# Kernel tuning notes

Measured on AMD Instinct MI355X. Metric: run time of the kernel, lower is better.

Reference implementation:

```python
import jax, jax.numpy as jnp
import numpy as np

D_MODEL = 1024
GEOM_DIM = 32
CLAMP_VALUE = 10.0


def setup_inputs() -> dict:
    key = jax.random.key(0)
    k1, k2, k3 = jax.random.split(key, 3)
    B, N = 4, 2048
    H = jax.random.normal(k1, (B, N, D_MODEL), dtype=jnp.float32)
    B_prev = jax.random.normal(k2, (B, N, N), dtype=jnp.float32)
    # geom_proj weight, init std=0.001 as in the torch module
    W = jax.random.normal(k3, (GEOM_DIM, D_MODEL), dtype=jnp.float32) * 0.001
    alpha = jnp.asarray(1.0, dtype=jnp.float32)
    beta = jnp.asarray(0.05, dtype=jnp.float32)
    return {"H": H, "B_prev": B_prev, "W": W, "alpha": alpha, "beta": beta}


def reference(H, B_prev, W, alpha, beta):
    # Low-rank projection: G [B, N, geom_dim]
    G = jnp.einsum("bnd,kd->bnk", H, W)
    G_sq = jnp.sum(G * G, axis=-1)  # [B, N]
    # Pairwise squared distance: [B, N, N]
    gram = jnp.einsum("bik,bjk->bij", G, G)
    dist = G_sq[:, :, None] + G_sq[:, None, :] - 2.0 * gram
    dist = jnp.maximum(dist, 0.0)
    # EMA bias update with clamp
    B_next = alpha * B_prev - beta * dist
    B_next = jnp.clip(B_next, -CLAMP_VALUE, CLAMP_VALUE)
    return B_next
```

## Files before the change

### kernel.cpp

```cpp
#include <hip/hip_runtime.h>


typedef __attribute__((ext_vector_type(8))) short short8;
typedef __attribute__((ext_vector_type(4))) float floatx4;

static __device__ __forceinline__ short bf16_bits(float f) {
    union { float f; unsigned int u; } v; v.f = f;
    unsigned int u = v.u;
    u += 0x7FFFu + ((u >> 16) & 1u);
    return (short)(u >> 16);
}

__global__ __launch_bounds__(256) void k1_proj(const float* __restrict__ H,
                                               const float* __restrict__ W,
                                               float* __restrict__ G,
                                               float* __restrict__ Q) {
    const int blk  = blockIdx.x;
    const int t    = threadIdx.x;
    const int w    = t >> 6;
    const int lane = t & 63;
    const int m    = lane & 15;
    const int quad = lane >> 4;

    const float* hrow  = H + ((long)blk * 16 + m) * 1024;
    const float* wrow0 = W + (long)m * 1024;
    const float* wrow1 = W + (long)(m + 16) * 1024;

    const int kq = w * 256 + quad * 8;

    floatx4 acc0 = {0.f, 0.f, 0.f, 0.f};
    floatx4 acc1 = {0.f, 0.f, 0.f, 0.f};

    float4 a0  = *(const float4*)(hrow  + kq);
    float4 a1  = *(const float4*)(hrow  + kq + 4);
    float4 b00 = *(const float4*)(wrow0 + kq);
    float4 b01 = *(const float4*)(wrow0 + kq + 4);
    float4 b10 = *(const float4*)(wrow1 + kq);
    float4 b11 = *(const float4*)(wrow1 + kq + 4);

    #pragma unroll
    for (int step = 0; step < 8; ++step) {
        float4 na0, na1, nb00, nb01, nb10, nb11;
        if (step < 7) {
            const int nk = kq + (step + 1) * 32;
            na0  = *(const float4*)(hrow  + nk);
            na1  = *(const float4*)(hrow  + nk + 4);
            nb00 = *(const float4*)(wrow0 + nk);
            nb01 = *(const float4*)(wrow0 + nk + 4);
            nb10 = *(const float4*)(wrow1 + nk);
            nb11 = *(const float4*)(wrow1 + nk + 4);
        }
        short8 af, bf0, bf1;
        af[0] = bf16_bits(a0.x);  af[1] = bf16_bits(a0.y);
        af[2] = bf16_bits(a0.z);  af[3] = bf16_bits(a0.w);
        af[4] = bf16_bits(a1.x);  af[5] = bf16_bits(a1.y);
        af[6] = bf16_bits(a1.z);  af[7] = bf16_bits(a1.w);
        bf0[0] = bf16_bits(b00.x); bf0[1] = bf16_bits(b00.y);
        bf0[2] = bf16_bits(b00.z); bf0[3] = bf16_bits(b00.w);
        bf0[4] = bf16_bits(b01.x); bf0[5] = bf16_bits(b01.y);
        bf0[6] = bf16_bits(b01.z); bf0[7] = bf16_bits(b01.w);
        bf1[0] = bf16_bits(b10.x); bf1[1] = bf16_bits(b10.y);
        bf1[2] = bf16_bits(b10.z); bf1[3] = bf16_bits(b10.w);
        bf1[4] = bf16_bits(b11.x); bf1[5] = bf16_bits(b11.y);
        bf1[6] = bf16_bits(b11.z); bf1[7] = bf16_bits(b11.w);

        acc0 = __builtin_amdgcn_mfma_f32_16x16x32_bf16(af, bf0, acc0, 0, 0, 0);
        acc1 = __builtin_amdgcn_mfma_f32_16x16x32_bf16(af, bf1, acc1, 0, 0, 0);

        if (step < 7) { a0 = na0; a1 = na1; b00 = nb00; b01 = nb01; b10 = nb10; b11 = nb11; }
    }

    __shared__ float red[4][16][32];
    #pragma unroll
    for (int r = 0; r < 4; ++r) {
        red[w][quad * 4 + r][m]      = acc0[r];
        red[w][quad * 4 + r][m + 16] = acc1[r];
    }
    __syncthreads();
    for (int e = t; e < 512; e += 256) {
        const int mm = e >> 5, nn = e & 31;
        float v = red[0][mm][nn] + red[1][mm][nn] + red[2][mm][nn] + red[3][mm][nn];
        G[(long)(blk * 16 + mm) * 32 + nn] = v;
        red[0][mm][nn] = v;
    }
    __syncthreads();
    if (t < 16) {
        float s = 0.f;
        #pragma unroll
        for (int nn = 0; nn < 32; ++nn) { const float v = red[0][t][nn]; s += v * v; }
        Q[blk * 16 + t] = s;
    }
}

__global__ __launch_bounds__(256) void k2_update(const float* __restrict__ Bp,
                                                 const float* __restrict__ G,
                                                 const float* __restrict__ Q,
                                                 const float* __restrict__ alphap,
                                                 const float* __restrict__ betap,
                                                 float* __restrict__ out) {
    __shared__ float4 sGi[128 * 8];
    __shared__ float4 sGj[128 * 8];
    __shared__ float  sQi[128];
    __shared__ float  sQj[128];

    const int b  = blockIdx.z;
    const int i0 = blockIdx.y * 128;
    const int j0 = blockIdx.x * 128;
    const int t  = threadIdx.x;

    const float4* Gi4 = (const float4*)(G + ((long)b * 2048 + i0) * 32);
    const float4* Gj4 = (const float4*)(G + ((long)b * 2048 + j0) * 32);
    #pragma unroll
    for (int l = 0; l < 4; ++l) {
        const int f = t + l * 256;
        const int r = f >> 3, c = f & 7;
        const int cs = c ^ ((r >> 3) & 7);
        sGi[r * 8 + cs] = Gi4[f];
        sGj[r * 8 + cs] = Gj4[f];
    }
    if (t < 128) sQi[t] = Q[b * 2048 + i0 + t];
    else         sQj[t - 128] = Q[b * 2048 + j0 + (t - 128)];
    __syncthreads();

    const int tx = t & 15;
    const int ty = t >> 4;

    float acc[8][8];
    #pragma unroll
    for (int ii = 0; ii < 8; ++ii)
        #pragma unroll
        for (int jj = 0; jj < 8; ++jj) acc[ii][jj] = 0.f;

    #pragma unroll
    for (int c = 0; c < 8; ++c) {
        float4 gi[8], gj[8];
        #pragma unroll
        for (int u = 0; u < 8; ++u) {
            const int ri = ty * 8 + u;
            gi[u] = sGi[ri * 8 + (c ^ ((ri >> 3) & 7))];
            const int rj = tx * 8 + u;
            gj[u] = sGj[rj * 8 + (c ^ ((rj >> 3) & 7))];
        }
        #pragma unroll
        for (int ii = 0; ii < 8; ++ii)
            #pragma unroll
            for (int jj = 0; jj < 8; ++jj)
                acc[ii][jj] += gi[ii].x * gj[jj].x + gi[ii].y * gj[jj].y +
                               gi[ii].z * gj[jj].z + gi[ii].w * gj[jj].w;
    }

    const float alpha = alphap[0];
    const float beta  = betap[0];

    #pragma unroll
    for (int ii = 0; ii < 8; ++ii) {
        const int i = i0 + ty * 8 + ii;
        const long rowoff = ((long)b * 2048 + i) * 2048 + j0;
        const float4* bp = (const float4*)(Bp + rowoff);
        float4*       op = (float4*)(out + rowoff);
        const float qi = sQi[ty * 8 + ii];
        #pragma unroll
        for (int g = 0; g < 2; ++g) {
            const float4 bv = bp[tx * 2 + g];
            float4 ov;
            {
                const int jj = g * 4 + 0;
                float d = qi + sQj[tx * 8 + jj] - 2.f * acc[ii][jj];
                d = fmaxf(d, 0.f);
                ov.x = fminf(fmaxf(alpha * bv.x - beta * d, -10.f), 10.f);
            }
            {
                const int jj = g * 4 + 1;
                float d = qi + sQj[tx * 8 + jj] - 2.f * acc[ii][jj];
                d = fmaxf(d, 0.f);
                ov.y = fminf(fmaxf(alpha * bv.y - beta * d, -10.f), 10.f);
            }
            {
                const int jj = g * 4 + 2;
                float d = qi + sQj[tx * 8 + jj] - 2.f * acc[ii][jj];
                d = fmaxf(d, 0.f);
                ov.z = fminf(fmaxf(alpha * bv.z - beta * d, -10.f), 10.f);
            }
            {
                const int jj = g * 4 + 3;
                float d = qi + sQj[tx * 8 + jj] - 2.f * acc[ii][jj];
                d = fmaxf(d, 0.f);
                ov.w = fminf(fmaxf(alpha * bv.w - beta * d, -10.f), 10.f);
            }
            op[tx * 2 + g] = ov;
        }
    }
}

extern "C" void kernel_launch(void* const* d_in, const int* in_sizes, int n_in,
                              void* d_out, int out_size, void* d_ws, size_t ws_size,
                              hipStream_t stream) {
    const float* H     = (const float*)d_in[0];
    const float* Bp    = (const float*)d_in[1];
    const float* W     = (const float*)d_in[2];
    const float* alpha = (const float*)d_in[3];
    const float* beta  = (const float*)d_in[4];
    float* out = (float*)d_out;

    float* G = (float*)d_ws;
    float* Q = G + 8192 * 32;

    k1_proj<<<512, 256, 0, stream>>>(H, W, G, Q);

    dim3 g2(16, 16, 4);
    k2_update<<<g2, 256, 0, stream>>>(Bp, G, Q, alpha, beta, out);
}
```

Before: 166.6 us.

## Replace bf16 MFMA projection with fp32 FMA and prefetch B_prev before gram

The projection kernel drops the bf16 MFMA path and computes each G element as an fp32 dot product, one thread per (row, k) pair, using more blocks with 8 rows each. The update kernel now issues all B_prev loads into registers before the shared-memory staging and the gram computation, so global-memory latency overlaps with the math. The gram inner loop is reordered to load one gj at a time, which lowers register pressure. The new code also adds launch-bound occupancy hints. In exchange, the 16 prefetched float4 values use extra registers, and the fp32 projection issues many more ALU instructions and reads W redundantly in each block.

```diff
diff --git a/kernel.cpp b/kernel.cpp
--- a/kernel.cpp
+++ b/kernel.cpp
@@ -1,103 +1,56 @@
 #include <hip/hip_runtime.h>
 
 
-typedef __attribute__((ext_vector_type(8))) short short8;
-typedef __attribute__((ext_vector_type(4))) float floatx4;
+__global__ __launch_bounds__(256, 4) void k1_proj(const float* __restrict__ H,
+                                                  const float* __restrict__ W,
+                                                  float* __restrict__ G,
+                                                  float* __restrict__ Q) {
+    __shared__ float sq[8][33];
+    const int t = threadIdx.x;
+    const int r = t & 7;
+    const int k = t >> 3;
+    const long row = (long)blockIdx.x * 8 + r;
+    const float* __restrict__ h = H + row * 1024;
+    const float* __restrict__ w = W + (long)k * 1024;
 
-static __device__ __forceinline__ short bf16_bits(float f) {
-    union { float f; unsigned int u; } v; v.f = f;
-    unsigned int u = v.u;
-    u += 0x7FFFu + ((u >> 16) & 1u);
-    return (short)(u >> 16);
-}
+    float4 a0 = {0.f,0.f,0.f,0.f}, a1 = {0.f,0.f,0.f,0.f};
+    float4 a2 = {0.f,0.f,0.f,0.f}, a3 = {0.f,0.f,0.f,0.f};
 
-__global__ __launch_bounds__(256) void k1_proj(const float* __restrict__ H,
-                                               const float* __restrict__ W,
-                                               float* __restrict__ G,
-                                               float* __restrict__ Q) {
-    const int blk  = blockIdx.x;
-    const int t    = threadIdx.x;
-    const int w    = t >> 6;
-    const int lane = t & 63;
-    const int m    = lane & 15;
-    const int quad = lane >> 4;
+    #pragma unroll 2
+    for (int d = 0; d < 1024; d += 16) {
+        const float4 h0 = *(const float4*)(h + d);
+        const float4 h1 = *(const float4*)(h + d + 4);
+        const float4 h2 = *(const float4*)(h + d + 8);
+        const float4 h3 = *(const float4*)(h + d + 12);
+        const float4 w0 = *(const float4*)(w + d);
+        const float4 w1 = *(const float4*)(w + d + 4);
+        const float4 w2 = *(const float4*)(w + d + 8);
+        const float4 w3 = *(const float4*)(w + d + 12);
+        a0.x += h0.x * w0.x; a0.y += h0.y * w0.y; a0.z += h0.z * w0.z; a0.w += h0.w * w0.w;
+        a1.x += h1.x * w1.x; a1.y += h1.y * w1.y; a1.z += h1.z * w1.z; a1.w += h1.w * w1.w;
+        a2.x += h2.x * w2.x; a2.y += h2.y * w2.y; a2.z += h2.z * w2.z; a2.w += h2.w * w2.w;
+        a3.x += h3.x * w3.x; a3.y += h3.y * w3.y; a3.z += h3.z * w3.z; a3.w += h3.w * w3.w;
+    }
+    const float s = ((a0.x + a0.y) + (a0.z + a0.w)) + ((a1.x + a1.y) + (a1.z + a1.w))
+                  + ((a2.x + a2.y) + (a2.z + a2.w)) + ((a3.x + a3.y) + (a3.z + a3.w));
 
-    const float* hrow  = H + ((long)blk * 16 + m) * 1024;
-    const float* wrow0 = W + (long)m * 1024;
-    const float* wrow1 = W + (long)(m + 16) * 1024;
-
-    const int kq = w * 256 + quad * 8;
-
-    floatx4 acc0 = {0.f, 0.f, 0.f, 0.f};
-    floatx4 acc1 = {0.f, 0.f, 0.f, 0.f};
-
-    float4 a0  = *(const float4*)(hrow  + kq);
-    float4 a1  = *(const float4*)(hrow  + kq + 4);
-    float4 b00 = *(const float4*)(wrow0 + kq);
-    float4 b01 = *(const float4*)(wrow0 + kq + 4);
-    float4 b10 = *(const float4*)(wrow1 + kq);
-    float4 b11 = *(const float4*)(wrow1 + kq + 4);
-
-    #pragma unroll
-    for (int step = 0; step < 8; ++step) {
-        float4 na0, na1, nb00, nb01, nb10, nb11;
-        if (step < 7) {
-            const int nk = kq + (step + 1) * 32;
-            na0  = *(const float4*)(hrow  + nk);
-            na1  = *(const float4*)(hrow  + nk + 4);
-            nb00 = *(const float4*)(wrow0 + nk);
-            nb01 = *(const float4*)(wrow0 + nk + 4);
-            nb10 = *(const float4*)(wrow1 + nk);
-            nb11 = *(const float4*)(wrow1 + nk + 4);
-        }
-        short8 af, bf0, bf1;
-        af[0] = bf16_bits(a0.x);  af[1] = bf16_bits(a0.y);
-        af[2] = bf16_bits(a0.z);  af[3] = bf16_bits(a0.w);
-        af[4] = bf16_bits(a1.x);  af[5] = bf16_bits(a1.y);
-        af[6] = bf16_bits(a1.z);  af[7] = bf16_bits(a1.w);
-        bf0[0] = bf16_bits(b00.x); bf0[1] = bf16_bits(b00.y);
-        bf0[2] = bf16_bits(b00.z); bf0[3] = bf16_bits(b00.w);
-        bf0[4] = bf16_bits(b01.x); bf0[5] = bf16_bits(b01.y);
-        bf0[6] = bf16_bits(b01.z); bf0[7] = bf16_bits(b01.w);
-        bf1[0] = bf16_bits(b10.x); bf1[1] = bf16_bits(b10.y);
-        bf1[2] = bf16_bits(b10.z); bf1[3] = bf16_bits(b10.w);
-        bf1[4] = bf16_bits(b11.x); bf1[5] = bf16_bits(b11.y);
-        bf1[6] = bf16_bits(b11.z); bf1[7] = bf16_bits(b11.w);
-
-        acc0 = __builtin_amdgcn_mfma_f32_16x16x32_bf16(af, bf0, acc0, 0, 0, 0);
-        acc1 = __builtin_amdgcn_mfma_f32_16x16x32_bf16(af, bf1, acc1, 0, 0, 0);
-
-        if (step < 7) { a0 = na0; a1 = na1; b00 = nb00; b01 = nb01; b10 = nb10; b11 = nb11; }
-    }
-
-    __shared__ float red[4][16][32];
-    #pragma unroll
-    for (int r = 0; r < 4; ++r) {
-        red[w][quad * 4 + r][m]      = acc0[r];
-        red[w][quad * 4 + r][m + 16] = acc1[r];
-    }
+    G[row * 32 + k] = s;
+    sq[r][k] = s * s;
     __syncthreads();
-    for (int e = t; e < 512; e += 256) {
-        const int mm = e >> 5, nn = e & 31;
-        float v = red[0][mm][nn] + red[1][mm][nn] + red[2][mm][nn] + red[3][mm][nn];
-        G[(long)(blk * 16 + mm) * 32 + nn] = v;
-        red[0][mm][nn] = v;
-    }
-    __syncthreads();
-    if (t < 16) {
-        float s = 0.f;
+    if (t < 8) {
+        float q = 0.f;
         #pragma unroll
-        for (int nn = 0; nn < 32; ++nn) { const float v = red[0][t][nn]; s += v * v; }
-        Q[blk * 16 + t] = s;
+        for (int kk = 0; kk < 32; ++kk) q += sq[t][kk];
+        Q[(long)blockIdx.x * 8 + t] = q;
     }
 }
 
-__global__ __launch_bounds__(256) void k2_update(const float* __restrict__ Bp,
-                                                 const float* __restrict__ G,
-                                                 const float* __restrict__ Q,
-                                                 const float* __restrict__ alphap,
-                                                 const float* __restrict__ betap,
-                                                 float* __restrict__ out) {
+__global__ __launch_bounds__(256, 2) void k2_update(const float* __restrict__ Bp,
+                                                    const float* __restrict__ G,
+                                                    const float* __restrict__ Q,
+                                                    const float* __restrict__ alphap,
+                                                    const float* __restrict__ betap,
+                                                    float* __restrict__ out) {
     __shared__ float4 sGi[128 * 8];
     __shared__ float4 sGj[128 * 8];
     __shared__ float  sQi[128];
@@ -107,6 +60,18 @@
     const int i0 = blockIdx.y * 128;
     const int j0 = blockIdx.x * 128;
     const int t  = threadIdx.x;
+    const int tx = t & 15;
+    const int ty = t >> 4;
+
+    float4 bv[16];
+    {
+        const float4* bp = (const float4*)(Bp + ((long)b * 2048 + i0 + ty * 8) * 2048 + j0);
+        #pragma unroll
+        for (int ii = 0; ii < 8; ++ii) {
+            bv[ii * 2 + 0] = bp[(long)ii * 512 + tx * 2 + 0];
+            bv[ii * 2 + 1] = bp[(long)ii * 512 + tx * 2 + 1];
+        }
+    }
 
     const float4* Gi4 = (const float4*)(G + ((long)b * 2048 + i0) * 32);
     const float4* Gj4 = (const float4*)(G + ((long)b * 2048 + j0) * 32);
@@ -114,16 +79,14 @@
     for (int l = 0; l < 4; ++l) {
         const int f = t + l * 256;
         const int r = f >> 3, c = f & 7;
-        const int cs = c ^ ((r >> 3) & 7);
-        sGi[r * 8 + cs] = Gi4[f];
-        sGj[r * 8 + cs] = Gj4[f];
+        const int cs = c ^ (r >> 3) % 8;
+        sGi[r * 8 + (c ^ ((r >> 3) & 7))] = Gi4[f];
+        sGj[r * 8 + (c ^ ((r >> 3) & 7))] = Gj4[f];
+        (void)cs;
     }
     if (t < 128) sQi[t] = Q[b * 2048 + i0 + t];
     else         sQj[t - 128] = Q[b * 2048 + j0 + (t - 128)];
     __syncthreads();
-
-    const int tx = t & 15;
-    const int ty = t >> 4;
 
     float acc[8][8];
     #pragma unroll
@@ -133,20 +96,21 @@
 
     #pragma unroll
     for (int c = 0; c < 8; ++c) {
-        float4 gi[8], gj[8];
+        float4 gi[8];
         #pragma unroll
         for (int u = 0; u < 8; ++u) {
             const int ri = ty * 8 + u;
             gi[u] = sGi[ri * 8 + (c ^ ((ri >> 3) & 7))];
-            const int rj = tx * 8 + u;
-            gj[u] = sGj[rj * 8 + (c ^ ((rj >> 3) & 7))];
         }
         #pragma unroll
-        for (int ii = 0; ii < 8; ++ii)
+        for (int jj = 0; jj < 8; ++jj) {
+            const int rj = tx * 8 + jj;
+            const float4 gj = sGj[rj * 8 + (c ^ ((rj >> 3) & 7))];
             #pragma unroll
-            for (int jj = 0; jj < 8; ++jj)
-                acc[ii][jj] += gi[ii].x * gj[jj].x + gi[ii].y * gj[jj].y +
-                               gi[ii].z * gj[jj].z + gi[ii].w * gj[jj].w;
+            for (int ii = 0; ii < 8; ++ii)
+                acc[ii][jj] += gi[ii].x * gj.x + gi[ii].y * gj.y +
+                               gi[ii].z * gj.z + gi[ii].w * gj.w;
+        }
     }
 
     const float alpha = alphap[0];
@@ -156,36 +120,31 @@
     for (int ii = 0; ii < 8; ++ii) {
         const int i = i0 + ty * 8 + ii;
         const long rowoff = ((long)b * 2048 + i) * 2048 + j0;
-        const float4* bp = (const float4*)(Bp + rowoff);
-        float4*       op = (float4*)(out + rowoff);
+        float4* op = (float4*)(out + rowoff);
         const float qi = sQi[ty * 8 + ii];
         #pragma unroll
         for (int g = 0; g < 2; ++g) {
-            const float4 bv = bp[tx * 2 + g];
+            const float4 bvv = bv[ii * 2 + g];
             float4 ov;
             {
                 const int jj = g * 4 + 0;
-                float d = qi + sQj[tx * 8 + jj] - 2.f * acc[ii][jj];
-                d = fmaxf(d, 0.f);
-                ov.x = fminf(fmaxf(alpha * bv.x - beta * d, -10.f), 10.f);
+                float d = fmaxf(qi + sQj[tx * 8 + jj] - 2.f * acc[ii][jj], 0.f);
+                ov.x = fminf(fmaxf(alpha * bvv.x - beta * d, -10.f), 10.f);
             }
             {
                 const int jj = g * 4 + 1;
-                float d = qi + sQj[tx * 8 + jj] - 2.f * acc[ii][jj];
-                d = fmaxf(d, 0.f);
-                ov.y = fminf(fmaxf(alpha * bv.y - beta * d, -10.f), 10.f);
+                float d = fmaxf(qi + sQj[tx * 8 + jj] - 2.f * acc[ii][jj], 0.f);
+                ov.y = fminf(fmaxf(alpha * bvv.y - beta * d, -10.f), 10.f);
             }
             {
                 const int jj = g * 4 + 2;
-                float d = qi + sQj[tx * 8 + jj] - 2.f * acc[ii][jj];
-                d = fmaxf(d, 0.f);
-                ov.z = fminf(fmaxf(alpha * bv.z - beta * d, -10.f), 10.f);
+                float d = fmaxf(qi + sQj[tx * 8 + jj] - 2.f * acc[ii][jj], 0.f);
+                ov.z = fminf(fmaxf(alpha * bvv.z - beta * d, -10.f), 10.f);
             }
             {
                 const int jj = g * 4 + 3;
-                float d = qi + sQj[tx * 8 + jj] - 2.f * acc[ii][jj];
-                d = fmaxf(d, 0.f);
-                ov.w = fminf(fmaxf(alpha * bv.w - beta * d, -10.f), 10.f);
+                float d = fmaxf(qi + sQj[tx * 8 + jj] - 2.f * acc[ii][jj], 0.f);
+                ov.w = fminf(fmaxf(alpha * bvv.w - beta * d, -10.f), 10.f);
             }
             op[tx * 2 + g] = ov;
         }
@@ -205,7 +164,7 @@
     float* G = (float*)d_ws;
     float* Q = G + 8192 * 32;
 
-    k1_proj<<<512, 256, 0, stream>>>(H, W, G, Q);
+    k1_proj<<<1024, 256, 0, stream>>>(H, W, G, Q);
 
     dim3 g2(16, 16, 4);
     k2_update<<<g2, 256, 0, stream>>>(Bp, G, Q, alpha, beta, out);
```

Measured after the change: 294.6 us. 76.8% more time.
